# Kernel tuning notes

Hardware: AMD Instinct MI355X
Metric: run time of the kernel (lower is better)

The kernel has to match this reference:

```python
import jax, jax.numpy as jnp
import numpy as np


def setup_inputs() -> dict:
    key = jax.random.key(0)
    k1, k2 = jax.random.split(key)
    B, S, K, N = 2, 4096, 4096, 4096
    x = jax.random.randint(k1, (B, S, K), -127, 128, dtype=jnp.int32).astype(jnp.int8)
    weight = jax.random.randint(k2, (N, K), -127, 128, dtype=jnp.int32).astype(jnp.int8)
    bias = jnp.zeros((1, N), dtype=jnp.int8)
    a = jnp.float32(0.01)   # alpha = input_scale * weight_scale / output_scale
    b = jnp.float32(1.0)    # beta = bias_scale / output_scale
    return {"x": x, "weight": weight, "bias": bias, "a": a, "b": b}


def reference(x, weight, bias, a, b):
    # i8gemm.linear_a8_w8_b8_o8: int8 GEMM with int32 accumulation, then
    # y_int8 = saturate_cast(round(alpha * acc + beta * bias)).
    x_shape = x.shape
    xf = x.reshape(-1, x_shape[-1])                     # [M, K] int8
    acc = jnp.matmul(xf, weight.T, preferred_element_type=jnp.int32)  # [M, N]
    y = a * acc.astype(jnp.float32) + b * bias.astype(jnp.float32)    # fused epilogue
    yq = jnp.clip(jnp.round(y), -128.0, 127.0).astype(jnp.int8)       # requantize o8
    return yq.reshape(*x_shape[:-1], -1)
```

## Files before the change

kernel.cpp:

```cpp
#include <hip/hip_runtime.h>
#include <stdint.h>

#define M_DIM 8192
#define N_DIM 4096
#define K_DIM 4096

using int4v = __attribute__((ext_vector_type(4))) int;

__device__ __forceinline__ unsigned int pack4(int4 v) {
    return (v.x & 0xff) | ((v.y & 0xff) << 8) | ((v.z & 0xff) << 16) |
           ((v.w & 0xff) << 24);
}

__global__ __launch_bounds__(256) void pack_kernel(const int4* __restrict__ src,
                                                   uint4* __restrict__ dst,
                                                   int n16) {
    int idx = blockIdx.x * blockDim.x + threadIdx.x;
    if (idx >= n16) return;
    int4 a = src[4 * idx + 0];
    int4 b = src[4 * idx + 1];
    int4 c = src[4 * idx + 2];
    int4 d = src[4 * idx + 3];
    dst[idx] = make_uint4(pack4(a), pack4(b), pack4(c), pack4(d));
}

__device__ __forceinline__ void async_copy16(const char* g, char* l) {
    __builtin_amdgcn_global_load_lds(
        (const __attribute__((address_space(1))) char*)g,
        (__attribute__((address_space(3))) char*)l, 16, 0, 0);
}

__global__ __launch_bounds__(256, 2) void gemm_i8_kernel(
    const char* __restrict__ Aq,
    const char* __restrict__ Bq,
    const int* __restrict__ bias,
    const float* __restrict__ a_ptr,
    const float* __restrict__ b_ptr,
    int32_t* __restrict__ out)
{
    __shared__ char As[128 * 64];
    __shared__ char Bs[128 * 64];

    const int tid  = threadIdx.x;
    const int lane = tid & 63;
    const int wave = tid >> 6;
    const int wr   = wave >> 1;
    const int wc   = wave & 1;
    const int m0   = blockIdx.y * 128;
    const int n0   = blockIdx.x * 128;

    const float alpha = *a_ptr;
    const float beta  = *b_ptr;

    int4v acc[4][4] = {};

    const int srow = tid >> 2;
    const int scol = (tid & 3) * 16;

    const char* aG0 = Aq + (size_t)(m0 + srow) * K_DIM + scol;
    const char* aG1 = aG0 + (size_t)64 * K_DIM;
    const char* bG0 = Bq + (size_t)(n0 + srow) * K_DIM + scol;
    const char* bG1 = bG0 + (size_t)64 * K_DIM;
    char* aL0 = &As[tid * 16];
    char* aL1 = &As[tid * 16 + 4096];
    char* bL0 = &Bs[tid * 16];
    char* bL1 = &Bs[tid * 16 + 4096];

    const int fr = lane & 15;
    const int fk = (lane >> 4) * 16;

    for (int k0 = 0; k0 < K_DIM; k0 += 64) {
        async_copy16(aG0 + k0, aL0);
        async_copy16(aG1 + k0, aL1);
        async_copy16(bG0 + k0, bL0);
        async_copy16(bG1 + k0, bL1);
        __syncthreads();

        int4v af[4], bf[4];
#pragma unroll
        for (int i = 0; i < 4; ++i)
            af[i] = *(const int4v*)&As[(wr * 64 + i * 16 + fr) * 64 + fk];
#pragma unroll
        for (int j = 0; j < 4; ++j)
            bf[j] = *(const int4v*)&Bs[(wc * 64 + j * 16 + fr) * 64 + fk];

#pragma unroll
        for (int i = 0; i < 4; ++i)
#pragma unroll
            for (int j = 0; j < 4; ++j)
                acc[i][j] = __builtin_amdgcn_mfma_i32_16x16x64_i8(
                    af[i], bf[j], acc[i][j], 0, 0, 0);

        __syncthreads();
    }

    const int orow = (lane >> 4) * 4;
    const int ocol = lane & 15;
#pragma unroll
    for (int j = 0; j < 4; ++j) {
        const int gn = n0 + wc * 64 + j * 16 + ocol;
        const float bb = beta * (float)bias[gn];
#pragma unroll
        for (int i = 0; i < 4; ++i) {
            const int gm = m0 + wr * 64 + i * 16 + orow;
#pragma unroll
            for (int r = 0; r < 4; ++r) {
                float v = alpha * (float)acc[i][j][r] + bb;
                v = rintf(v);
                v = fminf(fmaxf(v, -128.0f), 127.0f);
                out[(size_t)(gm + r) * N_DIM + gn] = (int32_t)v;
            }
        }
    }
}

extern "C" void kernel_launch(void* const* d_in, const int* in_sizes, int n_in,
                              void* d_out, int out_size, void* d_ws, size_t ws_size,
                              hipStream_t stream) {
    const int*   x    = (const int*)d_in[0];
    const int*   w    = (const int*)d_in[1];
    const int*   bias = (const int*)d_in[2];
    const float* a    = (const float*)d_in[3];
    const float* b    = (const float*)d_in[4];
    int32_t*     out  = (int32_t*)d_out;

    char* xq = (char*)d_ws;
    char* wq = xq + (size_t)M_DIM * K_DIM;

    const int n16x = (M_DIM * K_DIM) / 16;
    pack_kernel<<<n16x / 256, 256, 0, stream>>>((const int4*)x, (uint4*)xq, n16x);
    const int n16w = (N_DIM * K_DIM) / 16;
    pack_kernel<<<n16w / 256, 256, 0, stream>>>((const int4*)w, (uint4*)wq, n16w);

    dim3 grid(N_DIM / 128, M_DIM / 128);
    gemm_i8_kernel<<<grid, 256, 0, stream>>>(xq, wq, bias, a, b, out);
}
```

Baseline: 421.1 us.

## Switch GEMM to 32x32x32 int8 MFMA and merge pack kernels into one launch

Replaces the 16x16x64 int8 MFMA tiling with 32x32x32 MFMA tiles (2x2 per wave, two k-steps per 64-wide slice), which cuts the number of LDS fragment loads per MFMA and uses the larger, more efficient MFMA shape. The epilogue is remapped to the 32x32 accumulator row layout. The two int32->int8 pack launches are fused into a single kernel covering both x and weight, with each thread now packing 4 values instead of 16. That saves a launch but may lower per-thread memory efficiency in the packing step.

```diff
diff --git a/kernel.cpp b/kernel.cpp
--- a/kernel.cpp
+++ b/kernel.cpp
@@ -5,23 +5,18 @@
 #define N_DIM 4096
 #define K_DIM 4096
 
-using int4v = __attribute__((ext_vector_type(4))) int;
+using int4v  = __attribute__((ext_vector_type(4))) int;
+using int16v = __attribute__((ext_vector_type(16))) int;
 
-__device__ __forceinline__ unsigned int pack4(int4 v) {
-    return (v.x & 0xff) | ((v.y & 0xff) << 8) | ((v.z & 0xff) << 16) |
-           ((v.w & 0xff) << 24);
-}
-
-__global__ __launch_bounds__(256) void pack_kernel(const int4* __restrict__ src,
-                                                   uint4* __restrict__ dst,
-                                                   int n16) {
+__global__ __launch_bounds__(256) void pack_kernel(const int4* __restrict__ sx,
+                                                   const int4* __restrict__ sw,
+                                                   unsigned int* __restrict__ dst,
+                                                   int nx, int ntot) {
     int idx = blockIdx.x * blockDim.x + threadIdx.x;
-    if (idx >= n16) return;
-    int4 a = src[4 * idx + 0];
-    int4 b = src[4 * idx + 1];
-    int4 c = src[4 * idx + 2];
-    int4 d = src[4 * idx + 3];
-    dst[idx] = make_uint4(pack4(a), pack4(b), pack4(c), pack4(d));
+    if (idx >= ntot) return;
+    int4 v = (idx < nx) ? sx[idx] : sw[idx - nx];
+    dst[idx] = (v.x & 0xff) | ((v.y & 0xff) << 8) | ((v.z & 0xff) << 16) |
+               ((v.w & 0xff) << 24);
 }
 
 __device__ __forceinline__ void async_copy16(const char* g, char* l) {
@@ -52,7 +47,7 @@
     const float alpha = *a_ptr;
     const float beta  = *b_ptr;
 
-    int4v acc[4][4] = {};
+    int16v acc[2][2] = {};
 
     const int srow = tid >> 2;
     const int scol = (tid & 3) * 16;
@@ -66,8 +61,8 @@
     char* bL0 = &Bs[tid * 16];
     char* bL1 = &Bs[tid * 16 + 4096];
 
-    const int fr = lane & 15;
-    const int fk = (lane >> 4) * 16;
+    const int fm = lane & 31;
+    const int fk = (lane >> 5) * 16;
 
     for (int k0 = 0; k0 < K_DIM; k0 += 64) {
         async_copy16(aG0 + k0, aL0);
@@ -76,39 +71,45 @@
         async_copy16(bG1 + k0, bL1);
         __syncthreads();
 
-        int4v af[4], bf[4];
+        int4v af[2][2], bf[2][2];
 #pragma unroll
-        for (int i = 0; i < 4; ++i)
-            af[i] = *(const int4v*)&As[(wr * 64 + i * 16 + fr) * 64 + fk];
+        for (int i = 0; i < 2; ++i)
 #pragma unroll
-        for (int j = 0; j < 4; ++j)
-            bf[j] = *(const int4v*)&Bs[(wc * 64 + j * 16 + fr) * 64 + fk];
+            for (int kk = 0; kk < 2; ++kk) {
+                af[i][kk] = *(const int4v*)
+                    &As[(wr * 64 + i * 32 + fm) * 64 + kk * 32 + fk];
+                bf[i][kk] = *(const int4v*)
+                    &Bs[(wc * 64 + i * 32 + fm) * 64 + kk * 32 + fk];
+            }
 
 #pragma unroll
-        for (int i = 0; i < 4; ++i)
+        for (int i = 0; i < 2; ++i)
 #pragma unroll
-            for (int j = 0; j < 4; ++j)
-                acc[i][j] = __builtin_amdgcn_mfma_i32_16x16x64_i8(
-                    af[i], bf[j], acc[i][j], 0, 0, 0);
+            for (int j = 0; j < 2; ++j)
+#pragma unroll
+                for (int kk = 0; kk < 2; ++kk)
+                    acc[i][j] = __builtin_amdgcn_mfma_i32_32x32x32_i8(
+                        af[i][kk], bf[j][kk], acc[i][j], 0, 0, 0);
 
         __syncthreads();
     }
 
-    const int orow = (lane >> 4) * 4;
-    const int ocol = lane & 15;
+    const int ocol  = lane & 31;
+    const int rbase = (lane >> 5) * 4;
 #pragma unroll
-    for (int j = 0; j < 4; ++j) {
-        const int gn = n0 + wc * 64 + j * 16 + ocol;
+    for (int j = 0; j < 2; ++j) {
+        const int gn = n0 + wc * 64 + j * 32 + ocol;
         const float bb = beta * (float)bias[gn];
 #pragma unroll
-        for (int i = 0; i < 4; ++i) {
-            const int gm = m0 + wr * 64 + i * 16 + orow;
+        for (int i = 0; i < 2; ++i) {
+            const int gm = m0 + wr * 64 + i * 32;
 #pragma unroll
-            for (int r = 0; r < 4; ++r) {
+            for (int r = 0; r < 16; ++r) {
+                const int row = (r & 3) + 8 * (r >> 2) + rbase;
                 float v = alpha * (float)acc[i][j][r] + bb;
                 v = rintf(v);
                 v = fminf(fmaxf(v, -128.0f), 127.0f);
-                out[(size_t)(gm + r) * N_DIM + gn] = (int32_t)v;
+                out[(size_t)(gm + row) * N_DIM + gn] = (int32_t)v;
             }
         }
     }
@@ -125,12 +126,13 @@
     int32_t*     out  = (int32_t*)d_out;
 
     char* xq = (char*)d_ws;
+    const int nx   = (M_DIM * K_DIM) / 4;
+    const int nw   = (N_DIM * K_DIM) / 4;
+    const int ntot = nx + nw;
+    pack_kernel<<<(ntot + 255) / 256, 256, 0, stream>>>(
+        (const int4*)x, (const int4*)w, (unsigned int*)xq, nx, ntot);
+
     char* wq = xq + (size_t)M_DIM * K_DIM;
-
-    const int n16x = (M_DIM * K_DIM) / 16;
-    pack_kernel<<<n16x / 256, 256, 0, stream>>>((const int4*)x, (uint4*)xq, n16x);
-    const int n16w = (N_DIM * K_DIM) / 16;
-    pack_kernel<<<n16w / 256, 256, 0, stream>>>((const int4*)w, (uint4*)wq, n16w);
 
     dim3 grid(N_DIM / 128, M_DIM / 128);
     gemm_i8_kernel<<<grid, 256, 0, stream>>>(xq, wq, bias, a, b, out);
```

New measurement: 429.6 us. 1.02x slower.

## Double-buffer LDS tiles with prefetch and merge the two pack kernels

Applied to the files above, without the earlier changes.

The GEMM main loop now uses two LDS buffers for the A and B tiles. The next K-tile is issued via global_load_lds right after the barrier, so it loads while MFMAs run on the current tile, and one of the two barriers per iteration is dropped. The separate x and weight int32-to-int8 pack launches are merged into one launch, with each thread packing 4 bytes instead of 16. This doubles LDS use per block and narrows the pack kernel's per-thread stores.

```diff
diff --git a/kernel.cpp b/kernel.cpp
--- a/kernel.cpp
+++ b/kernel.cpp
@@ -7,21 +7,15 @@
 
 using int4v = __attribute__((ext_vector_type(4))) int;
 
-__device__ __forceinline__ unsigned int pack4(int4 v) {
-    return (v.x & 0xff) | ((v.y & 0xff) << 8) | ((v.z & 0xff) << 16) |
-           ((v.w & 0xff) << 24);
-}
-
-__global__ __launch_bounds__(256) void pack_kernel(const int4* __restrict__ src,
-                                                   uint4* __restrict__ dst,
-                                                   int n16) {
+__global__ __launch_bounds__(256) void pack_kernel(const int4* __restrict__ sx,
+                                                   const int4* __restrict__ sw,
+                                                   unsigned int* __restrict__ dst,
+                                                   int nx, int ntot) {
     int idx = blockIdx.x * blockDim.x + threadIdx.x;
-    if (idx >= n16) return;
-    int4 a = src[4 * idx + 0];
-    int4 b = src[4 * idx + 1];
-    int4 c = src[4 * idx + 2];
-    int4 d = src[4 * idx + 3];
-    dst[idx] = make_uint4(pack4(a), pack4(b), pack4(c), pack4(d));
+    if (idx >= ntot) return;
+    int4 v = (idx < nx) ? sx[idx] : sw[idx - nx];
+    dst[idx] = (v.x & 0xff) | ((v.y & 0xff) << 8) | ((v.z & 0xff) << 16) |
+               ((v.w & 0xff) << 24);
 }
 
 __device__ __forceinline__ void async_copy16(const char* g, char* l) {
@@ -38,8 +32,8 @@
     const float* __restrict__ b_ptr,
     int32_t* __restrict__ out)
 {
-    __shared__ char As[128 * 64];
-    __shared__ char Bs[128 * 64];
+    __shared__ char As[2][128 * 64];
+    __shared__ char Bs[2][128 * 64];
 
     const int tid  = threadIdx.x;
     const int lane = tid & 63;
@@ -61,28 +55,36 @@
     const char* aG1 = aG0 + (size_t)64 * K_DIM;
     const char* bG0 = Bq + (size_t)(n0 + srow) * K_DIM + scol;
     const char* bG1 = bG0 + (size_t)64 * K_DIM;
-    char* aL0 = &As[tid * 16];
-    char* aL1 = &As[tid * 16 + 4096];
-    char* bL0 = &Bs[tid * 16];
-    char* bL1 = &Bs[tid * 16 + 4096];
+    const int l0 = tid * 16;
+    const int l1 = tid * 16 + 4096;
 
     const int fr = lane & 15;
     const int fk = (lane >> 4) * 16;
 
+    async_copy16(aG0, &As[0][l0]);
+    async_copy16(aG1, &As[0][l1]);
+    async_copy16(bG0, &Bs[0][l0]);
+    async_copy16(bG1, &Bs[0][l1]);
+
+    int cur = 0;
     for (int k0 = 0; k0 < K_DIM; k0 += 64) {
-        async_copy16(aG0 + k0, aL0);
-        async_copy16(aG1 + k0, aL1);
-        async_copy16(bG0 + k0, bL0);
-        async_copy16(bG1 + k0, bL1);
         __syncthreads();
+
+        const int nxt = cur ^ 1;
+        if (k0 + 64 < K_DIM) {
+            async_copy16(aG0 + k0 + 64, &As[nxt][l0]);
+            async_copy16(aG1 + k0 + 64, &As[nxt][l1]);
+            async_copy16(bG0 + k0 + 64, &Bs[nxt][l0]);
+            async_copy16(bG1 + k0 + 64, &Bs[nxt][l1]);
+        }
 
         int4v af[4], bf[4];
 #pragma unroll
         for (int i = 0; i < 4; ++i)
-            af[i] = *(const int4v*)&As[(wr * 64 + i * 16 + fr) * 64 + fk];
+            af[i] = *(const int4v*)&As[cur][(wr * 64 + i * 16 + fr) * 64 + fk];
 #pragma unroll
         for (int j = 0; j < 4; ++j)
-            bf[j] = *(const int4v*)&Bs[(wc * 64 + j * 16 + fr) * 64 + fk];
+            bf[j] = *(const int4v*)&Bs[cur][(wc * 64 + j * 16 + fr) * 64 + fk];
 
 #pragma unroll
         for (int i = 0; i < 4; ++i)
@@ -91,7 +93,7 @@
                 acc[i][j] = __builtin_amdgcn_mfma_i32_16x16x64_i8(
                     af[i], bf[j], acc[i][j], 0, 0, 0);
 
-        __syncthreads();
+        cur = nxt;
     }
 
     const int orow = (lane >> 4) * 4;
@@ -125,12 +127,13 @@
     int32_t*     out  = (int32_t*)d_out;
 
     char* xq = (char*)d_ws;
+    const int nx   = (M_DIM * K_DIM) / 4;
+    const int nw   = (N_DIM * K_DIM) / 4;
+    const int ntot = nx + nw;
+    pack_kernel<<<(ntot + 255) / 256, 256, 0, stream>>>(
+        (const int4*)x, (const int4*)w, (unsigned int*)xq, nx, ntot);
+
     char* wq = xq + (size_t)M_DIM * K_DIM;
-
-    const int n16x = (M_DIM * K_DIM) / 16;
-    pack_kernel<<<n16x / 256, 256, 0, stream>>>((const int4*)x, (uint4*)xq, n16x);
-    const int n16w = (N_DIM * K_DIM) / 16;
-    pack_kernel<<<n16w / 256, 256, 0, stream>>>((const int4*)w, (uint4*)wq, n16w);
 
     dim3 grid(N_DIM / 128, M_DIM / 128);
     gemm_i8_kernel<<<grid, 256, 0, stream>>>(xq, wq, bias, a, b, out);
```

Result: faster. 409.2 us (-2.8%).
